# Performance work log

Measured on AMD Instinct MI355X. Metric: run time of the kernel, lower is better.

Reference implementation:

```python
import jax, jax.numpy as jnp
import numpy as np
from jax.scipy.special import logsumexp

COST_GAMMA = 0.1
MIN_ZERO_GAMMA = 0.1
_CLIP = 1.0 - 1e-7


def setup_inputs() -> dict:
    key = jax.random.key(0)
    k1, k2, k3 = jax.random.split(key, 3)
    B, D, K = 65536, 128, 1024
    xs = jax.random.normal(k1, (B, D), dtype=jnp.float32)
    xs = xs / jnp.linalg.norm(xs, axis=-1, keepdims=True)  # points on sphere S^{D-1}
    mus = jax.random.normal(k2, (D, K), dtype=jnp.float32)  # prototype params (pre-projx)
    alphas = jax.random.uniform(k3, (K,), dtype=jnp.float32)
    return {"xs": xs, "mus": mus, "alphas": alphas}


def reference(xs, mus, alphas):
    # projx: project prototype columns onto the unit sphere
    mus_p = mus / jnp.linalg.norm(mus, axis=0, keepdims=True)  # [D, K]
    # sphere cost: half squared geodesic distance, cdist-like [B, K]
    ip = jnp.clip(xs @ mus_p, -_CLIP, _CLIP)
    costs = 0.5 * jnp.arccos(ip) ** 2 + alphas  # [B, K]
    # softmin over components via stable logsumexp
    F = COST_GAMMA * logsumexp(-costs / COST_GAMMA, axis=1)  # [B]
    # soft min(F, 0): logsumexp over stacked (F, 0) == logaddexp
    F = MIN_ZERO_GAMMA * jnp.logaddexp(-F / MIN_ZERO_GAMMA, 0.0)
    return F
```

## Files before the change

### kernel.cpp

```cpp
#include <hip/hip_runtime.h>
#include <hip/hip_bf16.h>


typedef __attribute__((ext_vector_type(8))) short short8;
typedef __attribute__((ext_vector_type(4))) float f32x4;

#define KP 1024
#define DD 128

__device__ __forceinline__ unsigned int f2bf(float f) {
  unsigned int u = __float_as_uint(f);
  return (u + 0x7FFFu + ((u >> 16) & 1u)) >> 16;
}

__global__ __launch_bounds__(256) void prep_kernel(
    const float* __restrict__ xs, const float* __restrict__ mus,
    const float* __restrict__ alphas, unsigned short* __restrict__ abf,
    unsigned short* __restrict__ musbf, float* __restrict__ w,
    float* __restrict__ S) {
  const int t = threadIdx.x;
  if (blockIdx.x < 32) {
    __shared__ float psum[8][32];
    __shared__ float Tt[32][129];
    __shared__ float inv_s[32];
    const int k0 = blockIdx.x * 32;
    const int kk = t & 31, gg = t >> 5;
    float s = 0.0f;
    for (int i = 0; i < 16; ++i) {
      float v = mus[(gg * 16 + i) * KP + k0 + kk];
      s = fmaf(v, v, s);
    }
    psum[gg][kk] = s;
    __syncthreads();
    if (t < 32) {
      float tot = 0.0f;
      for (int j = 0; j < 8; ++j) tot += psum[j][t];
      inv_s[t] = rsqrtf(tot);
      w[k0 + t] = __expf(-10.0f * alphas[k0 + t]);
    }
    for (int i = 0; i < 16; ++i) {
      int e = i * 256 + t;
      Tt[e & 31][e >> 5] = mus[(e >> 5) * KP + k0 + (e & 31)];
    }
    __syncthreads();
    for (int i = 0; i < 8; ++i) {
      int o = i * 256 + t;
      int kx = o >> 6, dp = o & 63;
      float inv = inv_s[kx];
      float a = Tt[kx][2 * dp] * inv;
      float b = Tt[kx][2 * dp + 1] * inv;
      ((unsigned int*)musbf)[(k0 + kx) * (DD / 2) + dp] =
          f2bf(a) | (f2bf(b) << 16);
    }
  } else {
    const int xb = blockIdx.x - 32;
    if (xb < 256) S[xb * 256 + t] = 0.0f;
    const int u = xb * 256 + t;
    const int mtile = u >> 8, kkk = (u >> 6) & 3, ln = u & 63;
    const int row = mtile * 16 + (ln & 15), col = kkk * 32 + (ln >> 4) * 8;
    const float4* p = (const float4*)(xs + (size_t)row * DD + col);
    float4 f0 = p[0], f1 = p[1];
    uint4 o;
    o.x = f2bf(f0.x) | (f2bf(f0.y) << 16);
    o.y = f2bf(f0.z) | (f2bf(f0.w) << 16);
    o.z = f2bf(f1.x) | (f2bf(f1.y) << 16);
    o.w = f2bf(f1.z) | (f2bf(f1.w) << 16);
    ((uint4*)abf)[u] = o;
  }
}

__global__ __launch_bounds__(256, 3) void main_kernel(
    const unsigned short* __restrict__ abf,
    const unsigned short* __restrict__ musbf,
    const float* __restrict__ w, float* __restrict__ S) {
  __shared__ float Spart[512];
  const int t = threadIdx.x;
  const int wv = t >> 6, ln = t & 63, q = ln >> 4, l15 = ln & 15;
  const int b = blockIdx.x;
  const int g = (b >> 3) & 7;
  const int rowchunk = (b & 7) + ((b >> 6) << 3);
  const int mt_half = wv >> 1, col_half = wv & 1;
  const int cbase = g * 128 + col_half * 64;

  Spart[t] = 0.0f;
  Spart[t + 256] = 0.0f;
  __syncthreads();

  short8 bfrag[4][4];
  float wn[4];
  #pragma unroll
  for (int nt = 0; nt < 4; ++nt) {
    const int colr = cbase + nt * 16 + l15;
    wn[nt] = w[colr];
    const unsigned short* bp = musbf + colr * DD + q * 8;
    #pragma unroll
    for (int kkk = 0; kkk < 4; ++kkk)
      bfrag[nt][kkk] = *(const short8*)(bp + kkk * 32);
  }

  const int r0 = rowchunk * 512;
  const unsigned short* ap =
      abf + (size_t)(rowchunk * 32 + mt_half) * 2048 + ln * 8;

  for (int it = 0; it < 16; ++it) {
    short8 afr[4];
    #pragma unroll
    for (int kkk = 0; kkk < 4; ++kkk)
      afr[kkk] = *(const short8*)(ap + kkk * 512);

    f32x4 acc[4];
    #pragma unroll
    for (int nt = 0; nt < 4; ++nt) acc[nt] = (f32x4){0.f, 0.f, 0.f, 0.f};
    #pragma unroll
    for (int kkk = 0; kkk < 4; ++kkk)
      #pragma unroll
      for (int nt = 0; nt < 4; ++nt)
        acc[nt] = __builtin_amdgcn_mfma_f32_16x16x32_bf16(
            afr[kkk], bfrag[nt][kkk], acc[nt], 0, 0, 0);

    float sums[4] = {0.f, 0.f, 0.f, 0.f};
    #pragma unroll
    for (int nt = 0; nt < 4; ++nt) {
      #pragma unroll
      for (int r = 0; r < 4; ++r) {
        float x = acc[nt][r];
        float z = fmaxf(fmaf(x, -0.5f, 0.5f), 0.0f);
        float h = fmaf(z, -3.6067376f, -2.3449500f);
        h = fmaf(z, h, -3.2975886f);
        h = fmaf(z, h, -5.1295823f);
        h = fmaf(z, h, -9.6179669f);
        h = fmaf(z, h, -28.8539008f);
        float e = __builtin_amdgcn_exp2f(z * h);
        sums[r] = fmaf(e, wn[nt], sums[r]);
      }
    }
    #pragma unroll
    for (int s = 1; s < 16; s <<= 1)
      #pragma unroll
      for (int r = 0; r < 4; ++r) sums[r] += __shfl_xor(sums[r], s, 64);
    if (l15 == 0) {
      const int base = it * 32 + mt_half * 16 + q * 4;
      #pragma unroll
      for (int r = 0; r < 4; ++r) atomicAdd(&Spart[base + r], sums[r]);
    }
    ap += 4096;
  }

  __syncthreads();
  atomicAdd(&S[r0 + t], Spart[t]);
  atomicAdd(&S[r0 + 256 + t], Spart[t + 256]);
}

__global__ __launch_bounds__(256) void finalize_kernel(
    const float* __restrict__ S, float* __restrict__ out) {
  const int i = blockIdx.x * 256 + threadIdx.x;
  out[i] = 0.1f * log1pf(1.0f / S[i]);
}

extern "C" void kernel_launch(void* const* d_in, const int* in_sizes, int n_in,
                              void* d_out, int out_size, void* d_ws, size_t ws_size,
                              hipStream_t stream) {
  const float* xs     = (const float*)d_in[0];
  const float* mus    = (const float*)d_in[1];
  const float* alphas = (const float*)d_in[2];
  float* out = (float*)d_out;

  char* p = (char*)d_ws;
  unsigned short* abf   = (unsigned short*)p;
  unsigned short* musbf = (unsigned short*)(p + 16777216);
  float* w              = (float*)(p + 16777216 + 262144);
  float* S              = (float*)(p + 16777216 + 262144 + 4096);

  const int B = in_sizes[0] / DD;
  prep_kernel<<<32 + (B * DD / 8 + 255) / 256, 256, 0, stream>>>(
      xs, mus, alphas, abf, musbf, w, S);
  main_kernel<<<1024, 256, 0, stream>>>(abf, musbf, w, S);
  finalize_kernel<<<B / 256, 256, 0, stream>>>(S, out);
}
```

Before: 116.5 us.

## Fuse xs bf16 conversion and finalize into main kernel with LDS-staged prototypes

The main kernel now reads fp32 xs directly and converts it to bf16 fragments in registers, which removes the separate abf staging buffer and its 16 MB write/read round trip. Each block owns 64 full rows and loops over all 1024 prototypes, streaming 64-column prototype tiles through a double-buffered LDS region, so the row sum finishes in registers. That removes the global atomics, the S buffer and the finalize kernel. The costs are that every block rereads all prototype data from L2 and the loop now needs 15 block barriers. Launch bounds go from 3 to 4 waves.

```diff
diff --git a/kernel.cpp b/kernel.cpp
--- a/kernel.cpp
+++ b/kernel.cpp
@@ -14,113 +14,103 @@
 }
 
 __global__ __launch_bounds__(256) void prep_kernel(
-    const float* __restrict__ xs, const float* __restrict__ mus,
-    const float* __restrict__ alphas, unsigned short* __restrict__ abf,
-    unsigned short* __restrict__ musbf, float* __restrict__ w,
-    float* __restrict__ S) {
+    const float* __restrict__ mus, const float* __restrict__ alphas,
+    uint4* __restrict__ musbf_sw, float* __restrict__ w) {
+  __shared__ float psum[8][32];
+  __shared__ float Tt[32][129];
+  __shared__ float inv_s[32];
   const int t = threadIdx.x;
-  if (blockIdx.x < 32) {
-    __shared__ float psum[8][32];
-    __shared__ float Tt[32][129];
-    __shared__ float inv_s[32];
-    const int k0 = blockIdx.x * 32;
-    const int kk = t & 31, gg = t >> 5;
-    float s = 0.0f;
-    for (int i = 0; i < 16; ++i) {
-      float v = mus[(gg * 16 + i) * KP + k0 + kk];
-      s = fmaf(v, v, s);
-    }
-    psum[gg][kk] = s;
-    __syncthreads();
-    if (t < 32) {
-      float tot = 0.0f;
-      for (int j = 0; j < 8; ++j) tot += psum[j][t];
-      inv_s[t] = rsqrtf(tot);
-      w[k0 + t] = __expf(-10.0f * alphas[k0 + t]);
-    }
-    for (int i = 0; i < 16; ++i) {
-      int e = i * 256 + t;
-      Tt[e & 31][e >> 5] = mus[(e >> 5) * KP + k0 + (e & 31)];
-    }
-    __syncthreads();
-    for (int i = 0; i < 8; ++i) {
-      int o = i * 256 + t;
-      int kx = o >> 6, dp = o & 63;
-      float inv = inv_s[kx];
-      float a = Tt[kx][2 * dp] * inv;
-      float b = Tt[kx][2 * dp + 1] * inv;
-      ((unsigned int*)musbf)[(k0 + kx) * (DD / 2) + dp] =
-          f2bf(a) | (f2bf(b) << 16);
-    }
-  } else {
-    const int xb = blockIdx.x - 32;
-    if (xb < 256) S[xb * 256 + t] = 0.0f;
-    const int u = xb * 256 + t;
-    const int mtile = u >> 8, kkk = (u >> 6) & 3, ln = u & 63;
-    const int row = mtile * 16 + (ln & 15), col = kkk * 32 + (ln >> 4) * 8;
-    const float4* p = (const float4*)(xs + (size_t)row * DD + col);
-    float4 f0 = p[0], f1 = p[1];
+  const int k0 = blockIdx.x * 32;
+  const int kk = t & 31, gg = t >> 5;
+  float s = 0.0f;
+  for (int i = 0; i < 16; ++i) {
+    float v = mus[(gg * 16 + i) * KP + k0 + kk];
+    s = fmaf(v, v, s);
+  }
+  psum[gg][kk] = s;
+  __syncthreads();
+  if (t < 32) {
+    float tot = 0.0f;
+    for (int j = 0; j < 8; ++j) tot += psum[j][t];
+    inv_s[t] = rsqrtf(tot);
+    w[k0 + t] = __expf(-10.0f * alphas[k0 + t]);
+  }
+  for (int i = 0; i < 16; ++i) {
+    int e = i * 256 + t;
+    Tt[e & 31][e >> 5] = mus[(e >> 5) * KP + k0 + (e & 31)];
+  }
+  __syncthreads();
+  #pragma unroll
+  for (int i = 0; i < 2; ++i) {
+    int u = i * 256 + t;
+    int w0 = u >> 5, c32 = u & 31;
+    int col = k0 + c32;
+    float inv = inv_s[c32];
     uint4 o;
-    o.x = f2bf(f0.x) | (f2bf(f0.y) << 16);
-    o.y = f2bf(f0.z) | (f2bf(f0.w) << 16);
-    o.z = f2bf(f1.x) | (f2bf(f1.y) << 16);
-    o.w = f2bf(f1.z) | (f2bf(f1.w) << 16);
-    ((uint4*)abf)[u] = o;
+    o.x = f2bf(Tt[c32][w0 * 8 + 0] * inv) | (f2bf(Tt[c32][w0 * 8 + 1] * inv) << 16);
+    o.y = f2bf(Tt[c32][w0 * 8 + 2] * inv) | (f2bf(Tt[c32][w0 * 8 + 3] * inv) << 16);
+    o.z = f2bf(Tt[c32][w0 * 8 + 4] * inv) | (f2bf(Tt[c32][w0 * 8 + 5] * inv) << 16);
+    o.w = f2bf(Tt[c32][w0 * 8 + 6] * inv) | (f2bf(Tt[c32][w0 * 8 + 7] * inv) << 16);
+    musbf_sw[((col >> 6) << 10) + (w0 << 6) + (col & 63)] = o;
   }
 }
 
-__global__ __launch_bounds__(256, 3) void main_kernel(
-    const unsigned short* __restrict__ abf,
-    const unsigned short* __restrict__ musbf,
-    const float* __restrict__ w, float* __restrict__ S) {
-  __shared__ float Spart[512];
+__global__ __launch_bounds__(256, 4) void main_kernel(
+    const float* __restrict__ xs, const uint4* __restrict__ musbf_sw,
+    const float* __restrict__ w, float* __restrict__ out) {
+  __shared__ __align__(16) unsigned short Bs[2][8192];
   const int t = threadIdx.x;
   const int wv = t >> 6, ln = t & 63, q = ln >> 4, l15 = ln & 15;
-  const int b = blockIdx.x;
-  const int g = (b >> 3) & 7;
-  const int rowchunk = (b & 7) + ((b >> 6) << 3);
-  const int mt_half = wv >> 1, col_half = wv & 1;
-  const int cbase = g * 128 + col_half * 64;
 
-  Spart[t] = 0.0f;
-  Spart[t + 256] = 0.0f;
+  const int row = blockIdx.x * 64 + wv * 16 + l15;
+  const float4* xs4 = (const float4*)xs;
+  const int base4 = row * 32 + q * 2;
+  short8 afr[4];
+  #pragma unroll
+  for (int kkk = 0; kkk < 4; ++kkk) {
+    float4 f0 = xs4[base4 + kkk * 8];
+    float4 f1 = xs4[base4 + kkk * 8 + 1];
+    union { short8 s; uint4 u; } a;
+    a.u.x = f2bf(f0.x) | (f2bf(f0.y) << 16);
+    a.u.y = f2bf(f0.z) | (f2bf(f0.w) << 16);
+    a.u.z = f2bf(f1.x) | (f2bf(f1.y) << 16);
+    a.u.w = f2bf(f1.z) | (f2bf(f1.w) << 16);
+    afr[kkk] = a.s;
+  }
+
+  uint4 v[4];
+  #pragma unroll
+  for (int i = 0; i < 4; ++i) v[i] = musbf_sw[i * 256 + t];
+  #pragma unroll
+  for (int i = 0; i < 4; ++i) *(uint4*)&Bs[0][(i * 256 + t) * 8] = v[i];
   __syncthreads();
 
-  short8 bfrag[4][4];
-  float wn[4];
-  #pragma unroll
-  for (int nt = 0; nt < 4; ++nt) {
-    const int colr = cbase + nt * 16 + l15;
-    wn[nt] = w[colr];
-    const unsigned short* bp = musbf + colr * DD + q * 8;
+  float sums[4] = {0.f, 0.f, 0.f, 0.f};
+
+  for (int cg = 0; cg < 16; ++cg) {
+    if (cg < 15) {
+      #pragma unroll
+      for (int i = 0; i < 4; ++i)
+        v[i] = musbf_sw[(cg + 1) * 1024 + i * 256 + t];
+    }
+    float wn[4];
     #pragma unroll
-    for (int kkk = 0; kkk < 4; ++kkk)
-      bfrag[nt][kkk] = *(const short8*)(bp + kkk * 32);
-  }
-
-  const int r0 = rowchunk * 512;
-  const unsigned short* ap =
-      abf + (size_t)(rowchunk * 32 + mt_half) * 2048 + ln * 8;
-
-  for (int it = 0; it < 16; ++it) {
-    short8 afr[4];
-    #pragma unroll
-    for (int kkk = 0; kkk < 4; ++kkk)
-      afr[kkk] = *(const short8*)(ap + kkk * 512);
+    for (int nt = 0; nt < 4; ++nt) wn[nt] = w[cg * 64 + nt * 16 + l15];
 
     f32x4 acc[4];
     #pragma unroll
     for (int nt = 0; nt < 4; ++nt) acc[nt] = (f32x4){0.f, 0.f, 0.f, 0.f};
+    const unsigned short* bp = &Bs[cg & 1][q * 512 + l15 * 8];
     #pragma unroll
     for (int kkk = 0; kkk < 4; ++kkk)
       #pragma unroll
-      for (int nt = 0; nt < 4; ++nt)
-        acc[nt] = __builtin_amdgcn_mfma_f32_16x16x32_bf16(
-            afr[kkk], bfrag[nt][kkk], acc[nt], 0, 0, 0);
+      for (int nt = 0; nt < 4; ++nt) {
+        short8 b = *(const short8*)(bp + kkk * 2048 + nt * 128);
+        acc[nt] = __builtin_amdgcn_mfma_f32_16x16x32_bf16(afr[kkk], b, acc[nt], 0, 0, 0);
+      }
 
-    float sums[4] = {0.f, 0.f, 0.f, 0.f};
     #pragma unroll
-    for (int nt = 0; nt < 4; ++nt) {
+    for (int nt = 0; nt < 4; ++nt)
       #pragma unroll
       for (int r = 0; r < 4; ++r) {
         float x = acc[nt][r];
@@ -133,28 +123,24 @@
         float e = __builtin_amdgcn_exp2f(z * h);
         sums[r] = fmaf(e, wn[nt], sums[r]);
       }
+
+    if (cg < 15) {
+      #pragma unroll
+      for (int i = 0; i < 4; ++i)
+        *(uint4*)&Bs[(cg + 1) & 1][(i * 256 + t) * 8] = v[i];
+      __syncthreads();
     }
-    #pragma unroll
-    for (int s = 1; s < 16; s <<= 1)
-      #pragma unroll
-      for (int r = 0; r < 4; ++r) sums[r] += __shfl_xor(sums[r], s, 64);
-    if (l15 == 0) {
-      const int base = it * 32 + mt_half * 16 + q * 4;
-      #pragma unroll
-      for (int r = 0; r < 4; ++r) atomicAdd(&Spart[base + r], sums[r]);
-    }
-    ap += 4096;
   }
 
-  __syncthreads();
-  atomicAdd(&S[r0 + t], Spart[t]);
-  atomicAdd(&S[r0 + 256 + t], Spart[t + 256]);
-}
-
-__global__ __launch_bounds__(256) void finalize_kernel(
-    const float* __restrict__ S, float* __restrict__ out) {
-  const int i = blockIdx.x * 256 + threadIdx.x;
-  out[i] = 0.1f * log1pf(1.0f / S[i]);
+  #pragma unroll
+  for (int s2 = 1; s2 < 16; s2 <<= 1)
+    #pragma unroll
+    for (int r = 0; r < 4; ++r) sums[r] += __shfl_xor(sums[r], s2, 64);
+  if (l15 == 0) {
+    #pragma unroll
+    for (int r = 0; r < 4; ++r)
+      out[blockIdx.x * 64 + wv * 16 + q * 4 + r] = 0.1f * log1pf(1.0f / sums[r]);
+  }
 }
 
 extern "C" void kernel_launch(void* const* d_in, const int* in_sizes, int n_in,
@@ -165,15 +151,10 @@
   const float* alphas = (const float*)d_in[2];
   float* out = (float*)d_out;
 
-  char* p = (char*)d_ws;
-  unsigned short* abf   = (unsigned short*)p;
-  unsigned short* musbf = (unsigned short*)(p + 16777216);
-  float* w              = (float*)(p + 16777216 + 262144);
-  float* S              = (float*)(p + 16777216 + 262144 + 4096);
+  uint4* musbf_sw = (uint4*)d_ws;
+  float* w = (float*)((char*)d_ws + 16384 * sizeof(uint4));
 
+  prep_kernel<<<KP / 32, 256, 0, stream>>>(mus, alphas, musbf_sw, w);
   const int B = in_sizes[0] / DD;
-  prep_kernel<<<32 + (B * DD / 8 + 255) / 256, 256, 0, stream>>>(
-      xs, mus, alphas, abf, musbf, w, S);
-  main_kernel<<<1024, 256, 0, stream>>>(abf, musbf, w, S);
-  finalize_kernel<<<B / 256, 256, 0, stream>>>(S, out);
+  main_kernel<<<B / 64, 256, 0, stream>>>(xs, musbf_sw, w, out);
 }
```

Measured after the change: 110.2 us. -5.4%, faster.
